# Kernel tuning notes

Hardware: AMD Instinct MI355X
Metric: run time of the kernel (lower is better)

The kernel has to match this reference:

```python
import jax, jax.numpy as jnp
import numpy as np

B_, L_, D_, N_ = 4, 4096, 64, 16
DT = 0.1
EPS = 1e-6


def _complex_log(x):
    # log|x| (clamped) + i*pi for negative entries, matching torch impl
    real = jnp.log(jnp.maximum(jnp.abs(x), EPS))
    imag = jnp.where(x < 0, jnp.float32(np.pi), jnp.float32(0.0))
    return jax.lax.complex(real, imag)


def _clogaddexp(a, b):
    # stable complex log(exp(a)+exp(b)) using max of real parts
    m = jnp.maximum(a.real, b.real)
    return jnp.log(jnp.exp(a - m) + jnp.exp(b - m)) + m


def _clogcumsumexp(x, axis):
    return jax.lax.associative_scan(_clogaddexp, x, axis=axis)


def setup_inputs() -> dict:
    key = jax.random.key(0)
    ks = jax.random.split(key, 6)
    x = jax.random.normal(ks[0], (B_, L_, D_), jnp.float32)
    s = 1.0 / np.sqrt(D_)
    Wb = jax.random.uniform(ks[1], (N_, D_), jnp.float32, -s, s)
    bb = jax.random.uniform(ks[2], (N_,), jnp.float32, -s, s)
    Wc = jax.random.uniform(ks[3], (N_, D_), jnp.float32, -s, s)
    bc = jax.random.uniform(ks[4], (N_,), jnp.float32, -s, s)
    Wd = jax.random.uniform(ks[5], (1, D_), jnp.float32, -s, s)
    bd = jnp.zeros((1,), jnp.float32)
    # S4D-Real init: A_n = -(n+1), repeated over input_dim rows -> (D, N)
    A = jnp.tile(-(jnp.arange(N_, dtype=jnp.float32) + 1.0)[None, :], (D_, 1))
    return {"x": x, "A": A, "Wb": Wb, "bb": bb, "Wc": Wc, "bc": bc,
            "Wd": Wd, "bd": bd}


def reference(x, A, Wb, bb, Wc, bc, Wd, bd):
    # projections: (b,l,n)
    Bm = x @ Wb.T + bb
    Cm = x @ Wc.T + bc
    # delta network: softplus(linear(x)) + dt, broadcast to input_dim
    delta = jax.nn.softplus(x @ Wd.T + bd) + DT            # (b,l,1)
    dt = jnp.broadcast_to(delta, x.shape)                  # (b,l,d)
    # discretize
    tmp = A * dt[..., None]                                # (b,l,d,n)
    A_bar = jnp.exp(tmp)
    delta_B = jnp.einsum('bld,bln->bldn', dt, Bm)
    B_bar = (A_bar - 1.0) * delta_B / (tmp + EPS)
    term2 = B_bar * x[..., None]                           # (b,l,d,n)
    # parallel scan via complex log-cumsum-exp trick
    log_a = _complex_log(A_bar)
    log_b = _complex_log(term2)
    a_star = jnp.cumsum(log_a, axis=1)                     # (b,l,d,n) complex
    t = _clogcumsumexp(log_b - a_star, axis=1)
    scan = jnp.exp(a_star + t).real                        # (b,l,d,n)
    return jnp.sum(scan * Cm[:, :, None, :], axis=-1)      # (b,l,d)
```

## Files before the change

### kernel.cpp

```cpp
#include <hip/hip_runtime.h>

#define B_ 4
#define L_ 4096
#define D_ 64
#define N_ 16
#define CHUNK 16
#define NCHUNK (L_ / CHUNK)
#define TOTCHUNK (B_ * NCHUNK)

constexpr float DT_  = 0.1f;
constexpr float EPS_ = 1e-6f;

__global__ __launch_bounds__(64) void proj_scan_kernel(
    const float* __restrict__ x,  const float* __restrict__ A,
    const float* __restrict__ Wb, const float* __restrict__ bb,
    const float* __restrict__ Wc, const float* __restrict__ bc,
    const float* __restrict__ Wd, const float* __restrict__ bd,
    float* __restrict__ P, float* __restrict__ Cm,
    float* __restrict__ S, float* __restrict__ Cdec)
{
    const int gc    = blockIdx.x;
    const int batch = gc >> 8;
    const int c     = gc & (NCHUNK - 1);
    const int lane  = threadIdx.x;
    const int base0 = batch * L_ + c * CHUNK;

    __shared__ float xs[CHUNK * D_];
    __shared__ float ag[CHUNK * 32];

    const float4* xg  = (const float4*)(x + (size_t)base0 * D_);
    float4*       xsv = (float4*)xs;
    #pragma unroll
    for (int i = 0; i < 4; i++) xsv[i * 64 + lane] = xg[i * 64 + lane];

    const int o  = lane & 31;
    const int h2 = lane >> 5;
    float wreg[32];
    const float* Wrow = (o < 16) ? (Wb + o * D_) : (Wc + (o - 16) * D_);
    const float4* w4p = (const float4*)(Wrow + h2 * 32);
    #pragma unroll
    for (int j = 0; j < 8; j++) {
        float4 w4 = w4p[j];
        wreg[4*j+0] = w4.x; wreg[4*j+1] = w4.y;
        wreg[4*j+2] = w4.z; wreg[4*j+3] = w4.w;
    }
    const float wd   = Wd[lane];
    const float bd0  = bd[0];
    const float An   = A[lane & 15];
    const float bias = (o < 16) ? bb[o] : bc[o - 16];

    __syncthreads();

    float r[CHUNK];
    #pragma unroll
    for (int p = 0; p < CHUNK; p++) r[p] = xs[p * D_ + lane] * wd;
    #pragma unroll
    for (int m = 32; m >= 1; m >>= 1) {
        #pragma unroll
        for (int p = 0; p < CHUNK; p++) r[p] += __shfl_xor(r[p], m, 64);
    }
    float delta[CHUNK];
    #pragma unroll
    for (int p = 0; p < CHUNK; p++) {
        float z = r[p] + bd0;
        delta[p] = fmaxf(z, 0.0f) + log1pf(expf(-fabsf(z))) + DT_;
    }

    #pragma unroll
    for (int p = 0; p < CHUNK; p++) {
        float acc = 0.0f;
        const float4* xs4 = (const float4*)(xs + p * D_ + h2 * 32);
        #pragma unroll
        for (int j = 0; j < 8; j++) {
            float4 v = xs4[j];
            acc += v.x * wreg[4*j+0] + v.y * wreg[4*j+1]
                 + v.z * wreg[4*j+2] + v.w * wreg[4*j+3];
        }
        acc += __shfl_xor(acc, 32, 64);
        const int pp = base0 + p;
        if (lane < 16) {
            float Bm  = acc + bias;
            float tmp = An * delta[p];
            float a   = expf(tmp);
            float g   = (a - 1.0f) * delta[p] * Bm / (tmp + EPS_);
            ag[p * 32 + lane]      = a;
            ag[p * 32 + 16 + lane] = g;
            P[(size_t)pp * 32 + lane]      = a;
            P[(size_t)pp * 32 + 16 + lane] = g;
        } else if (lane < 32) {
            Cm[(size_t)pp * 16 + (lane - 16)] = acc + bias;
        }
    }
    __syncthreads();

    float h[N_], cum[N_];
    #pragma unroll
    for (int n = 0; n < N_; n++) { h[n] = 0.0f; cum[n] = 1.0f; }
    for (int s = 0; s < CHUNK; s++) {
        float xd = xs[s * D_ + lane];
        const float4* row = (const float4*)(ag + s * 32);
        #pragma unroll
        for (int q = 0; q < 4; q++) {
            float4 a4 = row[q];
            float4 g4 = row[4 + q];
            h[4*q+0] = a4.x * h[4*q+0] + g4.x * xd;  cum[4*q+0] *= a4.x;
            h[4*q+1] = a4.y * h[4*q+1] + g4.y * xd;  cum[4*q+1] *= a4.y;
            h[4*q+2] = a4.z * h[4*q+2] + g4.z * xd;  cum[4*q+2] *= a4.z;
            h[4*q+3] = a4.w * h[4*q+3] + g4.w * xd;  cum[4*q+3] *= a4.w;
        }
    }
    #pragma unroll
    for (int n = 0; n < N_; n++)
        S[(size_t)(gc * N_ + n) * D_ + lane] = h[n];
    if (lane == 0) {
        #pragma unroll
        for (int n = 0; n < N_; n++) Cdec[gc * N_ + n] = cum[n];
    }
}

__global__ __launch_bounds__(64) void combine(
    float* __restrict__ S, const float* __restrict__ Cdec)
{
    const int b = blockIdx.x >> 4;
    const int n = blockIdx.x & 15;
    const int d = threadIdx.x;
    const int cb = b * NCHUNK;

    float run = 0.0f;
    float sbuf[4], abuf[4];
    #pragma unroll
    for (int j = 0; j < 4; j++) {
        sbuf[j] = S[(size_t)((cb + j) * N_ + n) * D_ + d];
        abuf[j] = Cdec[(cb + j) * N_ + n];
    }
    for (int c = 0; c < NCHUNK; c += 4) {
        const int cn = (c + 4 < NCHUNK) ? c + 4 : c;
        float t[4], u[4];
        #pragma unroll
        for (int j = 0; j < 4; j++) {
            t[j] = S[(size_t)((cb + cn + j) * N_ + n) * D_ + d];
            u[j] = Cdec[(cb + cn + j) * N_ + n];
        }
        #pragma unroll
        for (int j = 0; j < 4; j++) {
            S[(size_t)((cb + c + j) * N_ + n) * D_ + d] = run;
            run = abuf[j] * run + sbuf[j];
        }
        #pragma unroll
        for (int j = 0; j < 4; j++) { sbuf[j] = t[j]; abuf[j] = u[j]; }
    }
}

__global__ __launch_bounds__(64) void scan_out(
    const float* __restrict__ x, const float* __restrict__ P,
    const float* __restrict__ Cmat, const float* __restrict__ S,
    float* __restrict__ out)
{
    const int gc    = blockIdx.x;
    const int batch = gc >> 8;
    const int c     = gc & (NCHUNK - 1);
    const int lane  = threadIdx.x;
    const int base0 = batch * L_ + c * CHUNK;

    __shared__ float xs[CHUNK * D_];
    __shared__ float ag[CHUNK * 32];
    __shared__ float cm[CHUNK * N_];

    const float4* xg  = (const float4*)(x + (size_t)base0 * D_);
    float4*       xsv = (float4*)xs;
    #pragma unroll
    for (int i = 0; i < 4; i++) xsv[i * 64 + lane] = xg[i * 64 + lane];
    const float4* pg  = (const float4*)(P + (size_t)base0 * 32);
    float4*       agv = (float4*)ag;
    #pragma unroll
    for (int i = 0; i < 2; i++) agv[i * 64 + lane] = pg[i * 64 + lane];
    const float4* cg  = (const float4*)(Cmat + (size_t)base0 * 16);
    float4*       cmv = (float4*)cm;
    cmv[lane] = cg[lane];
    __syncthreads();

    float h[N_];
    #pragma unroll
    for (int n = 0; n < N_; n++)
        h[n] = S[(size_t)(gc * N_ + n) * D_ + lane];

    for (int s = 0; s < CHUNK; s++) {
        float xd = xs[s * D_ + lane];
        const float4* row = (const float4*)(ag + s * 32);
        const float4* crw = (const float4*)(cm + s * 16);
        float acc = 0.0f;
        #pragma unroll
        for (int q = 0; q < 4; q++) {
            float4 a4 = row[q];
            float4 g4 = row[4 + q];
            float4 c4 = crw[q];
            h[4*q+0] = a4.x * h[4*q+0] + g4.x * xd;  acc += c4.x * h[4*q+0];
            h[4*q+1] = a4.y * h[4*q+1] + g4.y * xd;  acc += c4.y * h[4*q+1];
            h[4*q+2] = a4.z * h[4*q+2] + g4.z * xd;  acc += c4.z * h[4*q+2];
            h[4*q+3] = a4.w * h[4*q+3] + g4.w * xd;  acc += c4.w * h[4*q+3];
        }
        out[(size_t)(base0 + s) * D_ + lane] = acc;
    }
}

extern "C" void kernel_launch(void* const* d_in, const int* in_sizes, int n_in,
                              void* d_out, int out_size, void* d_ws, size_t ws_size,
                              hipStream_t stream)
{
    const float* x  = (const float*)d_in[0];
    const float* A  = (const float*)d_in[1];
    const float* Wb = (const float*)d_in[2];
    const float* bb = (const float*)d_in[3];
    const float* Wc = (const float*)d_in[4];
    const float* bc = (const float*)d_in[5];
    const float* Wd = (const float*)d_in[6];
    const float* bd = (const float*)d_in[7];
    float* out = (float*)d_out;

    float* P    = (float*)d_ws;
    float* Cm   = P  + (size_t)B_ * L_ * 32;
    float* S    = Cm + (size_t)B_ * L_ * 16;
    float* Cdec = S  + (size_t)TOTCHUNK * N_ * D_;

    proj_scan_kernel<<<TOTCHUNK, 64, 0, stream>>>(x, A, Wb, bb, Wc, bc, Wd, bd,
                                                  P, Cm, S, Cdec);
    combine<<<B_ * N_, 64, 0, stream>>>(S, Cdec);
    scan_out<<<TOTCHUNK, 64, 0, stream>>>(x, P, Cm, S, out);
}
```

Baseline: 108.0 us.

## Fuse cross-chunk combine into projection kernel via last-block atomic counter

Removes the separate combine kernel launch. Each block bumps a per-batch atomic counter after writing its chunk state, and the last 16 blocks of each batch spin until every chunk is done, then each runs the serial carry scan for one state index n. P and Cm writes are also staged in shared memory and stored as coalesced float4 vectors. The change adds a memset launch and spin-waiting, and it relies on the late blocks being scheduled while earlier ones finish; because only the last 16 arrivals wait, this should not deadlock.

```diff
diff --git a/kernel.cpp b/kernel.cpp
--- a/kernel.cpp
+++ b/kernel.cpp
@@ -11,13 +11,14 @@
 constexpr float DT_  = 0.1f;
 constexpr float EPS_ = 1e-6f;
 
-__global__ __launch_bounds__(64) void proj_scan_kernel(
+__global__ __launch_bounds__(64) void proj_scan_combine_kernel(
     const float* __restrict__ x,  const float* __restrict__ A,
     const float* __restrict__ Wb, const float* __restrict__ bb,
     const float* __restrict__ Wc, const float* __restrict__ bc,
     const float* __restrict__ Wd, const float* __restrict__ bd,
     float* __restrict__ P, float* __restrict__ Cm,
-    float* __restrict__ S, float* __restrict__ Cdec)
+    float* __restrict__ S, float* __restrict__ Cdec,
+    int* __restrict__ ctr)
 {
     const int gc    = blockIdx.x;
     const int batch = gc >> 8;
@@ -27,6 +28,7 @@
 
     __shared__ float xs[CHUNK * D_];
     __shared__ float ag[CHUNK * 32];
+    __shared__ float cm[CHUNK * N_];
 
     const float4* xg  = (const float4*)(x + (size_t)base0 * D_);
     float4*       xsv = (float4*)xs;
@@ -77,7 +79,6 @@
                  + v.z * wreg[4*j+2] + v.w * wreg[4*j+3];
         }
         acc += __shfl_xor(acc, 32, 64);
-        const int pp = base0 + p;
         if (lane < 16) {
             float Bm  = acc + bias;
             float tmp = An * delta[p];
@@ -85,13 +86,21 @@
             float g   = (a - 1.0f) * delta[p] * Bm / (tmp + EPS_);
             ag[p * 32 + lane]      = a;
             ag[p * 32 + 16 + lane] = g;
-            P[(size_t)pp * 32 + lane]      = a;
-            P[(size_t)pp * 32 + 16 + lane] = g;
         } else if (lane < 32) {
-            Cm[(size_t)pp * 16 + (lane - 16)] = acc + bias;
+            cm[p * 16 + (lane - 16)] = acc + bias;
         }
     }
     __syncthreads();
+
+    {
+        float4*       Pg   = (float4*)(P + (size_t)base0 * 32);
+        const float4* agv4 = (const float4*)ag;
+        Pg[lane]      = agv4[lane];
+        Pg[64 + lane] = agv4[64 + lane];
+        float4*       Cg   = (float4*)(Cm + (size_t)base0 * 16);
+        const float4* cmv4 = (const float4*)cm;
+        Cg[lane] = cmv4[lane];
+    }
 
     float h[N_], cum[N_];
     #pragma unroll
@@ -116,38 +125,44 @@
         #pragma unroll
         for (int n = 0; n < N_; n++) Cdec[gc * N_ + n] = cum[n];
     }
-}
-
-__global__ __launch_bounds__(64) void combine(
-    float* __restrict__ S, const float* __restrict__ Cdec)
-{
-    const int b = blockIdx.x >> 4;
-    const int n = blockIdx.x & 15;
-    const int d = threadIdx.x;
-    const int cb = b * NCHUNK;
-
-    float run = 0.0f;
-    float sbuf[4], abuf[4];
-    #pragma unroll
-    for (int j = 0; j < 4; j++) {
-        sbuf[j] = S[(size_t)((cb + j) * N_ + n) * D_ + d];
-        abuf[j] = Cdec[(cb + j) * N_ + n];
-    }
-    for (int c = 0; c < NCHUNK; c += 4) {
-        const int cn = (c + 4 < NCHUNK) ? c + 4 : c;
-        float t[4], u[4];
-        #pragma unroll
-        for (int j = 0; j < 4; j++) {
-            t[j] = S[(size_t)((cb + cn + j) * N_ + n) * D_ + d];
-            u[j] = Cdec[(cb + cn + j) * N_ + n];
-        }
-        #pragma unroll
-        for (int j = 0; j < 4; j++) {
-            S[(size_t)((cb + c + j) * N_ + n) * D_ + d] = run;
-            run = abuf[j] * run + sbuf[j];
-        }
-        #pragma unroll
-        for (int j = 0; j < 4; j++) { sbuf[j] = t[j]; abuf[j] = u[j]; }
+
+    __threadfence();
+    int old = 0;
+    if (lane == 0) old = atomicAdd(&ctr[batch], 1);
+    old = __shfl(old, 0, 64);
+
+    if (old >= NCHUNK - 16) {
+        const int nrole = old - (NCHUNK - 16);
+        while (__hip_atomic_load(&ctr[batch], __ATOMIC_ACQUIRE,
+                                 __HIP_MEMORY_SCOPE_AGENT) < NCHUNK) {}
+        __threadfence();
+
+        float*       baseS = S    + (size_t)(batch * NCHUNK * N_ + nrole) * D_ + lane;
+        const float* baseA = Cdec + batch * NCHUNK * N_ + nrole;
+
+        float run = 0.0f;
+        float sbuf[8], abuf[8];
+        #pragma unroll
+        for (int j = 0; j < 8; j++) {
+            sbuf[j] = baseS[(size_t)j * (N_ * D_)];
+            abuf[j] = baseA[j * N_];
+        }
+        for (int cc = 0; cc < NCHUNK; cc += 8) {
+            const int cn = (cc + 8 < NCHUNK) ? (cc + 8) : cc;
+            float t[8], u[8];
+            #pragma unroll
+            for (int j = 0; j < 8; j++) {
+                t[j] = baseS[(size_t)(cn + j) * (N_ * D_)];
+                u[j] = baseA[(cn + j) * N_];
+            }
+            #pragma unroll
+            for (int j = 0; j < 8; j++) {
+                baseS[(size_t)(cc + j) * (N_ * D_)] = run;
+                run = abuf[j] * run + sbuf[j];
+            }
+            #pragma unroll
+            for (int j = 0; j < 8; j++) { sbuf[j] = t[j]; abuf[j] = u[j]; }
+        }
     }
 }
 
@@ -221,9 +236,10 @@
     float* Cm   = P  + (size_t)B_ * L_ * 32;
     float* S    = Cm + (size_t)B_ * L_ * 16;
     float* Cdec = S  + (size_t)TOTCHUNK * N_ * D_;
-
-    proj_scan_kernel<<<TOTCHUNK, 64, 0, stream>>>(x, A, Wb, bb, Wc, bc, Wd, bd,
-                                                  P, Cm, S, Cdec);
-    combine<<<B_ * N_, 64, 0, stream>>>(S, Cdec);
+    int*   ctr  = (int*)(Cdec + (size_t)TOTCHUNK * N_);
+
+    hipMemsetAsync(ctr, 0, B_ * sizeof(int), stream);
+    proj_scan_combine_kernel<<<TOTCHUNK, 64, 0, stream>>>(
+        x, A, Wb, bb, Wc, bc, Wd, bd, P, Cm, S, Cdec, ctr);
     scan_out<<<TOTCHUNK, 64, 0, stream>>>(x, P, Cm, S, out);
 }
```

After: 154.2 us. 42.7% more time.

## Emit intra-chunk outputs in first pass and add carry correction afterward

Applied to the files above, without the earlier changes.

The first kernel now computes the zero-initial-state scan output for each chunk and writes it straight to out. It also stores per-chunk decay-weighted C coefficients (Wcor) so a light apply kernel can add the carried-in state contribution later. This removes the P and Cm workspace round trip and the second full recurrence over x. The combine kernel also prefetches 32 chunks at a time instead of 4, at the cost of more registers. The apply kernel reads and rewrites out, which adds one extra read-modify-write of the output.

```diff
diff --git a/kernel.cpp b/kernel.cpp
--- a/kernel.cpp
+++ b/kernel.cpp
@@ -16,8 +16,8 @@
     const float* __restrict__ Wb, const float* __restrict__ bb,
     const float* __restrict__ Wc, const float* __restrict__ bc,
     const float* __restrict__ Wd, const float* __restrict__ bd,
-    float* __restrict__ P, float* __restrict__ Cm,
-    float* __restrict__ S, float* __restrict__ Cdec)
+    float* __restrict__ S, float* __restrict__ Cdec,
+    float* __restrict__ Wcor, float* __restrict__ out)
 {
     const int gc    = blockIdx.x;
     const int batch = gc >> 8;
@@ -27,6 +27,8 @@
 
     __shared__ float xs[CHUNK * D_];
     __shared__ float ag[CHUNK * 32];
+    __shared__ float cm[CHUNK * N_];
+    __shared__ float wbuf[CHUNK * N_];
 
     const float4* xg  = (const float4*)(x + (size_t)base0 * D_);
     float4*       xsv = (float4*)xs;
@@ -77,7 +79,6 @@
                  + v.z * wreg[4*j+2] + v.w * wreg[4*j+3];
         }
         acc += __shfl_xor(acc, 32, 64);
-        const int pp = base0 + p;
         if (lane < 16) {
             float Bm  = acc + bias;
             float tmp = An * delta[p];
@@ -85,105 +86,15 @@
             float g   = (a - 1.0f) * delta[p] * Bm / (tmp + EPS_);
             ag[p * 32 + lane]      = a;
             ag[p * 32 + 16 + lane] = g;
-            P[(size_t)pp * 32 + lane]      = a;
-            P[(size_t)pp * 32 + 16 + lane] = g;
         } else if (lane < 32) {
-            Cm[(size_t)pp * 16 + (lane - 16)] = acc + bias;
-        }
-    }
-    __syncthreads();
-
-    float h[N_], cum[N_];
-    #pragma unroll
-    for (int n = 0; n < N_; n++) { h[n] = 0.0f; cum[n] = 1.0f; }
-    for (int s = 0; s < CHUNK; s++) {
-        float xd = xs[s * D_ + lane];
-        const float4* row = (const float4*)(ag + s * 32);
-        #pragma unroll
-        for (int q = 0; q < 4; q++) {
-            float4 a4 = row[q];
-            float4 g4 = row[4 + q];
-            h[4*q+0] = a4.x * h[4*q+0] + g4.x * xd;  cum[4*q+0] *= a4.x;
-            h[4*q+1] = a4.y * h[4*q+1] + g4.y * xd;  cum[4*q+1] *= a4.y;
-            h[4*q+2] = a4.z * h[4*q+2] + g4.z * xd;  cum[4*q+2] *= a4.z;
-            h[4*q+3] = a4.w * h[4*q+3] + g4.w * xd;  cum[4*q+3] *= a4.w;
-        }
-    }
-    #pragma unroll
-    for (int n = 0; n < N_; n++)
-        S[(size_t)(gc * N_ + n) * D_ + lane] = h[n];
-    if (lane == 0) {
-        #pragma unroll
-        for (int n = 0; n < N_; n++) Cdec[gc * N_ + n] = cum[n];
-    }
-}
-
-__global__ __launch_bounds__(64) void combine(
-    float* __restrict__ S, const float* __restrict__ Cdec)
-{
-    const int b = blockIdx.x >> 4;
-    const int n = blockIdx.x & 15;
-    const int d = threadIdx.x;
-    const int cb = b * NCHUNK;
-
-    float run = 0.0f;
-    float sbuf[4], abuf[4];
-    #pragma unroll
-    for (int j = 0; j < 4; j++) {
-        sbuf[j] = S[(size_t)((cb + j) * N_ + n) * D_ + d];
-        abuf[j] = Cdec[(cb + j) * N_ + n];
-    }
-    for (int c = 0; c < NCHUNK; c += 4) {
-        const int cn = (c + 4 < NCHUNK) ? c + 4 : c;
-        float t[4], u[4];
-        #pragma unroll
-        for (int j = 0; j < 4; j++) {
-            t[j] = S[(size_t)((cb + cn + j) * N_ + n) * D_ + d];
-            u[j] = Cdec[(cb + cn + j) * N_ + n];
-        }
-        #pragma unroll
-        for (int j = 0; j < 4; j++) {
-            S[(size_t)((cb + c + j) * N_ + n) * D_ + d] = run;
-            run = abuf[j] * run + sbuf[j];
-        }
-        #pragma unroll
-        for (int j = 0; j < 4; j++) { sbuf[j] = t[j]; abuf[j] = u[j]; }
-    }
-}
-
-__global__ __launch_bounds__(64) void scan_out(
-    const float* __restrict__ x, const float* __restrict__ P,
-    const float* __restrict__ Cmat, const float* __restrict__ S,
-    float* __restrict__ out)
-{
-    const int gc    = blockIdx.x;
-    const int batch = gc >> 8;
-    const int c     = gc & (NCHUNK - 1);
-    const int lane  = threadIdx.x;
-    const int base0 = batch * L_ + c * CHUNK;
-
-    __shared__ float xs[CHUNK * D_];
-    __shared__ float ag[CHUNK * 32];
-    __shared__ float cm[CHUNK * N_];
-
-    const float4* xg  = (const float4*)(x + (size_t)base0 * D_);
-    float4*       xsv = (float4*)xs;
-    #pragma unroll
-    for (int i = 0; i < 4; i++) xsv[i * 64 + lane] = xg[i * 64 + lane];
-    const float4* pg  = (const float4*)(P + (size_t)base0 * 32);
-    float4*       agv = (float4*)ag;
-    #pragma unroll
-    for (int i = 0; i < 2; i++) agv[i * 64 + lane] = pg[i * 64 + lane];
-    const float4* cg  = (const float4*)(Cmat + (size_t)base0 * 16);
-    float4*       cmv = (float4*)cm;
-    cmv[lane] = cg[lane];
+            cm[p * 16 + (lane - 16)] = acc + bias;
+        }
+    }
     __syncthreads();
 
     float h[N_];
     #pragma unroll
-    for (int n = 0; n < N_; n++)
-        h[n] = S[(size_t)(gc * N_ + n) * D_ + lane];
-
+    for (int n = 0; n < N_; n++) h[n] = 0.0f;
     for (int s = 0; s < CHUNK; s++) {
         float xd = xs[s * D_ + lane];
         const float4* row = (const float4*)(ag + s * 32);
@@ -201,6 +112,102 @@
         }
         out[(size_t)(base0 + s) * D_ + lane] = acc;
     }
+    #pragma unroll
+    for (int n = 0; n < N_; n++)
+        S[(size_t)(gc * N_ + n) * D_ + lane] = h[n];
+
+    if (lane < 16) {
+        float cumn = 1.0f;
+        for (int s = 0; s < CHUNK; s++) {
+            cumn *= ag[s * 32 + lane];
+            wbuf[s * 16 + lane] = cm[s * 16 + lane] * cumn;
+        }
+        Cdec[gc * N_ + lane] = cumn;
+    }
+    __syncthreads();
+    ((float4*)(Wcor + (size_t)base0 * 16))[lane] = ((const float4*)wbuf)[lane];
+}
+
+#define G_ 32
+__global__ __launch_bounds__(64) void combine(
+    float* __restrict__ S, const float* __restrict__ Cdec)
+{
+    const int b = blockIdx.x >> 4;
+    const int n = blockIdx.x & 15;
+    const int d = threadIdx.x;
+    const int cb = b * NCHUNK;
+
+    float*       baseS = S    + (size_t)(cb * N_ + n) * D_ + d;
+    const float* baseA = Cdec + cb * N_ + n;
+
+    float run = 0.0f;
+    float sbuf[G_], abuf[G_];
+    #pragma unroll
+    for (int j = 0; j < G_; j++) {
+        sbuf[j] = baseS[(size_t)j * (N_ * D_)];
+        abuf[j] = baseA[j * N_];
+    }
+    for (int cc = 0; cc < NCHUNK; cc += G_) {
+        const int cn = (cc + G_ < NCHUNK) ? (cc + G_) : cc;
+        float t[G_], u[G_];
+        #pragma unroll
+        for (int j = 0; j < G_; j++) {
+            t[j] = baseS[(size_t)(cn + j) * (N_ * D_)];
+            u[j] = baseA[(cn + j) * N_];
+        }
+        #pragma unroll
+        for (int j = 0; j < G_; j++) {
+            baseS[(size_t)(cc + j) * (N_ * D_)] = run;
+            run = abuf[j] * run + sbuf[j];
+        }
+        #pragma unroll
+        for (int j = 0; j < G_; j++) { sbuf[j] = t[j]; abuf[j] = u[j]; }
+    }
+}
+
+__global__ __launch_bounds__(64) void apply_kernel(
+    const float* __restrict__ Wcor, const float* __restrict__ S,
+    float* __restrict__ out)
+{
+    const int gc    = blockIdx.x;
+    const int batch = gc >> 8;
+    const int c     = gc & (NCHUNK - 1);
+    const int lane  = threadIdx.x;
+    const int base0 = batch * L_ + c * CHUNK;
+
+    __shared__ float wl[CHUNK * N_];
+
+    ((float4*)wl)[lane] = ((const float4*)(Wcor + (size_t)base0 * 16))[lane];
+
+    float hi[N_];
+    #pragma unroll
+    for (int n = 0; n < N_; n++)
+        hi[n] = S[(size_t)(gc * N_ + n) * D_ + lane];
+
+    float4 ov[4];
+    const float4* og = (const float4*)(out + (size_t)base0 * D_);
+    #pragma unroll
+    for (int i = 0; i < 4; i++) ov[i] = og[i * 64 + lane];
+
+    __syncthreads();
+
+    float acc[CHUNK];
+    #pragma unroll
+    for (int s = 0; s < CHUNK; s++) {
+        const float4* crw = (const float4*)(wl + s * 16);
+        float a = 0.0f;
+        #pragma unroll
+        for (int q = 0; q < 4; q++) {
+            float4 w4 = crw[q];
+            a += w4.x * hi[4*q+0] + w4.y * hi[4*q+1]
+               + w4.z * hi[4*q+2] + w4.w * hi[4*q+3];
+        }
+        acc[s] = a;
+    }
+
+    #pragma unroll
+    for (int s = 0; s < CHUNK; s++)
+        out[(size_t)(base0 + s) * D_ + lane] = out[(size_t)(base0 + s) * D_ + lane] + acc[s];
 }
 
 extern "C" void kernel_launch(void* const* d_in, const int* in_sizes, int n_in,
@@ -217,13 +224,12 @@
     const float* bd = (const float*)d_in[7];
     float* out = (float*)d_out;
 
-    float* P    = (float*)d_ws;
-    float* Cm   = P  + (size_t)B_ * L_ * 32;
-    float* S    = Cm + (size_t)B_ * L_ * 16;
-    float* Cdec = S  + (size_t)TOTCHUNK * N_ * D_;
+    float* S    = (float*)d_ws;
+    float* Cdec = S    + (size_t)TOTCHUNK * N_ * D_;
+    float* Wcor = Cdec + (size_t)TOTCHUNK * N_;
 
     proj_scan_kernel<<<TOTCHUNK, 64, 0, stream>>>(x, A, Wb, bb, Wc, bc, Wd, bd,
-                                                  P, Cm, S, Cdec);
+                                                  S, Cdec, Wcor, out);
     combine<<<B_ * N_, 64, 0, stream>>>(S, Cdec);
-    scan_out<<<TOTCHUNK, 64, 0, stream>>>(x, P, Cm, S, out);
-}
+    apply_kernel<<<TOTCHUNK, 64, 0, stream>>>(Wcor, S, out);
+}
```

Result: faster. 103.4 us (-4.3%).
